# Performance work log

Hardware: AMD Instinct MI355X
Metric: run time of the kernel (lower is better)

The kernel has to match this reference:

```python
import jax, jax.numpy as jnp
import numpy as np

NUM_LEVELS = 4
CODEBOOK_SIZE = 256
DIM = 128
B = 262144


def setup_inputs() -> dict:
    key = jax.random.key(0)
    kx, kc = jax.random.split(key)
    x = jax.random.normal(kx, (B, DIM), dtype=jnp.float32)
    codebooks = jax.random.normal(kc, (NUM_LEVELS, CODEBOOK_SIZE, DIM), dtype=jnp.float32)
    return {"x": x, "codebooks": codebooks}


def reference(x, codebooks):
    # Residual quantization: per level, nearest codebook entry (L2), gather,
    # accumulate recon, subtract from residual.
    residual = x
    recon = jnp.zeros_like(x)
    codes = []
    for l in range(NUM_LEVELS):
        cb = codebooks[l]  # (K, D)
        # argmin of ||r - c||^2 == argmin of -2 r.c + ||c||^2 (drop ||r||^2 term)
        dist = -2.0 * (residual @ cb.T) + jnp.sum(cb * cb, axis=-1)  # (B, K)
        idx = jnp.argmin(dist, axis=1)  # (B,)
        codes.append(idx)
        selected = cb[idx]  # (B, D)
        recon = recon + selected
        residual = residual - selected
    codes = jnp.stack(codes, axis=1)  # (B, num_levels)
    return recon, codes
```

## Files before the change

kernel.cpp:

```cpp
#include <hip/hip_runtime.h>
#include <float.h>

#define NLVL  4
#define KCB   256
#define DIMD  128
#define NROWS 262144
#define WROWS 16
#define MARGIN 0.5f
#define WLCAP 256
#define RING  8
#define ADV   6

typedef _Float16 half8  __attribute__((ext_vector_type(8)));
typedef float    floatx4 __attribute__((ext_vector_type(4)));

#define WSYNC() asm volatile("s_waitcnt lgkmcnt(0)" ::: "memory")
#define VMW(N)  asm volatile("s_waitcnt vmcnt(" #N ")" ::: "memory")

__device__ __forceinline__ void glds16(const void* g, void* l) {
    __builtin_amdgcn_global_load_lds(
        (const __attribute__((address_space(1))) unsigned int*)g,
        (__attribute__((address_space(3))) unsigned int*)l, 16, 0, 0);
}

__global__ __launch_bounds__(256) void rq_prep_kernel(const float* __restrict__ cb,
                                                      float* __restrict__ c2,
                                                      _Float16* __restrict__ cbh) {
    int e = blockIdx.x * 256 + threadIdx.x;
    const float4* p = (const float4*)(cb + (size_t)e * DIMD);
    _Float16* ho = cbh + (size_t)e * DIMD;
    float s = 0.f;
#pragma unroll
    for (int k = 0; k < DIMD / 4; ++k) {
        float4 v = p[k];
        s = fmaf(v.x, v.x, s);
        s = fmaf(v.y, v.y, s);
        s = fmaf(v.z, v.z, s);
        s = fmaf(v.w, v.w, s);
        ho[4 * k + 0] = (_Float16)v.x;
        ho[4 * k + 1] = (_Float16)v.y;
        ho[4 * k + 2] = (_Float16)v.z;
        ho[4 * k + 3] = (_Float16)v.w;
    }
    c2[e] = s;
}

__global__ __launch_bounds__(64, 3) void rq_main_kernel(const float* __restrict__ x,
                                                        const float* __restrict__ cb,
                                                        const float* __restrict__ c2g,
                                                        const _Float16* __restrict__ cbh,
                                                        float* __restrict__ out) {
    __shared__ __align__(16) char ring[RING * 1024];
    __shared__ unsigned int wl[WLCAP];
    __shared__ unsigned long long refine_key[WROWS];
    __shared__ int codes_lds[WROWS][4];
    __shared__ int wl_cnt;

    const int lane = threadIdx.x;
    const int q    = lane >> 4;
    const int c    = lane & 15;
    const int rowW = blockIdx.x * WROWS;
    const int lane_off = ((lane >> 2) << 8) | ((lane & 3) << 4);
    const char* cbh_b = (const char*)cbh;

#pragma unroll
    for (int g = 0; g < ADV; ++g) {
        const char* src = cbh_b + ((g >> 6) << 16) + (((g & 63) >> 2) << 12)
                        + ((g & 3) << 6) + lane_off;
        glds16(src, ring + ((g & (RING - 1)) << 10));
    }

    float res_[32];
#pragma unroll
    for (int s = 0; s < 4; ++s) {
        const float* px = x + (size_t)(rowW + c) * DIMD + s * 32 + q * 8;
        float4 u = *(const float4*)px;
        float4 v = *(const float4*)(px + 4);
        res_[s*8+0]=u.x; res_[s*8+1]=u.y; res_[s*8+2]=u.z; res_[s*8+3]=u.w;
        res_[s*8+4]=v.x; res_[s*8+5]=v.y; res_[s*8+6]=v.z; res_[s*8+7]=v.w;
    }
    if (lane == 0) wl_cnt = 0;
    if (lane < WROWS) refine_key[lane] = ~0ULL;
    WSYNC();

    for (int l = 0; l < NLVL; ++l) {
        half8 a[4];
#pragma unroll
        for (int s = 0; s < 4; ++s)
#pragma unroll
            for (int j = 0; j < 8; ++j)
                a[s][j] = (_Float16)res_[s * 8 + j];

        floatx4 acc[16];
#pragma unroll
        for (int t = 0; t < 16; ++t) acc[t] = (floatx4){0.f, 0.f, 0.f, 0.f};

#pragma unroll
        for (int w = 0; w < 64; ++w) {
            if      (w <  59) VMW(5);
            else if (w == 59) VMW(4);
            else if (w == 60) VMW(3);
            else if (w == 61) VMW(2);
            else if (w == 62) VMW(1);
            else              VMW(0);
            half8 b = *(const half8*)(ring + ((w & (RING - 1)) << 10) + (c << 6) + (q << 4));
            if (l < NLVL - 1 || w < 64 - ADV) {
                int g2 = l * 64 + w + ADV;
                const char* src = cbh_b + ((g2 >> 6) << 16) + (((g2 & 63) >> 2) << 12)
                                + ((g2 & 3) << 6) + lane_off;
                glds16(src, ring + ((g2 & (RING - 1)) << 10));
            }
            acc[w >> 2] = __builtin_amdgcn_mfma_f32_16x16x32_f16(a[w & 3], b, acc[w >> 2], 0, 0, 0);
        }

        float c2v[16];
#pragma unroll
        for (int t = 0; t < 16; ++t) c2v[t] = c2g[l * KCB + t * 16 + c];

#pragma unroll
        for (int r = 0; r < 4; ++r) {
            float bv = FLT_MAX; int be = 0;
#pragma unroll
            for (int t = 0; t < 16; ++t) {
                float d = c2v[t] - 2.f * acc[t][r];
                if (d < bv) { bv = d; be = t * 16 + c; }
            }
#pragma unroll
            for (int m = 1; m < 16; m <<= 1) {
                float ov = __shfl_xor(bv, m);
                int   oe = __shfl_xor(be, m);
                if (ov < bv || (ov == bv && oe < be)) { bv = ov; be = oe; }
            }
            float thr = bv + MARGIN;
            int cnt = 0;
#pragma unroll
            for (int t = 0; t < 16; ++t)
                cnt += (c2v[t] - 2.f * acc[t][r]) <= thr;
#pragma unroll
            for (int m = 1; m < 16; m <<= 1) cnt += __shfl_xor(cnt, m);

            int row_m = q * 4 + r;
            if (c == 0) codes_lds[row_m][l] = be;
            if (cnt >= 2) {
#pragma unroll
                for (int t = 0; t < 16; ++t) {
                    float d = c2v[t] - 2.f * acc[t][r];
                    if (d <= thr) {
                        int slot = atomicAdd(&wl_cnt, 1);
                        if (slot < WLCAP)
                            wl[slot] = ((unsigned)row_m << 8) | (unsigned)(t * 16 + c);
                    }
                }
            }
        }
        WSYNC();

        int n = wl_cnt; if (n > WLCAP) n = WLCAP;
        for (int i = 0; i < n; ++i) {
            unsigned int it = wl[i];
            int row_m = (int)(it >> 8), e = (int)(it & 255u);
            bool act = (c == row_m);
            float d = 0.f;
            if (act) {
                const float* cc = cb + ((size_t)l * KCB + e) * DIMD + q * 8;
#pragma unroll
                for (int s = 0; s < 4; ++s) {
                    float4 u = *(const float4*)(cc + s * 32);
                    float4 v = *(const float4*)(cc + s * 32 + 4);
                    d = fmaf(res_[s*8+0], u.x, d); d = fmaf(res_[s*8+1], u.y, d);
                    d = fmaf(res_[s*8+2], u.z, d); d = fmaf(res_[s*8+3], u.w, d);
                    d = fmaf(res_[s*8+4], v.x, d); d = fmaf(res_[s*8+5], v.y, d);
                    d = fmaf(res_[s*8+6], v.z, d); d = fmaf(res_[s*8+7], v.w, d);
                }
            }
            d += __shfl_xor(d, 16);
            d += __shfl_xor(d, 32);
            if (act && q == 0) {
                float dist = c2g[l * KCB + e] - 2.f * d;
                unsigned int ob = __float_as_uint(dist);
                ob = (ob & 0x80000000u) ? ~ob : (ob | 0x80000000u);
                unsigned long long key = ((unsigned long long)ob << 32) | (unsigned int)e;
                atomicMin(&refine_key[row_m], key);
            }
        }
        WSYNC();

        {
            unsigned long long k = refine_key[c];
            int idx = (k != ~0ULL) ? (int)(k & 0xFFFFFFFFULL) : codes_lds[c][l];
            if (q == 0) codes_lds[c][l] = idx;
            const float* cbase = cb + ((size_t)l * KCB + idx) * DIMD + q * 8;
#pragma unroll
            for (int s = 0; s < 4; ++s) {
                float4 u = *(const float4*)(cbase + s * 32);
                float4 v = *(const float4*)(cbase + s * 32 + 4);
                res_[s*8+0] -= u.x; res_[s*8+1] -= u.y;
                res_[s*8+2] -= u.z; res_[s*8+3] -= u.w;
                res_[s*8+4] -= v.x; res_[s*8+5] -= v.y;
                res_[s*8+6] -= v.z; res_[s*8+7] -= v.w;
            }
        }
        if (lane == 0) wl_cnt = 0;
        if (lane < WROWS) refine_key[lane] = ~0ULL;
        WSYNC();
    }

#pragma unroll
    for (int s = 0; s < 4; ++s) {
        const float* px = x + (size_t)(rowW + c) * DIMD + s * 32 + q * 8;
        float4 u = *(const float4*)px;
        float4 v = *(const float4*)(px + 4);
        float4 o0, o1;
        o0.x = u.x - res_[s*8+0]; o0.y = u.y - res_[s*8+1];
        o0.z = u.z - res_[s*8+2]; o0.w = u.w - res_[s*8+3];
        o1.x = v.x - res_[s*8+4]; o1.y = v.y - res_[s*8+5];
        o1.z = v.z - res_[s*8+6]; o1.w = v.w - res_[s*8+7];
        float* po = out + (size_t)(rowW + c) * DIMD + s * 32 + q * 8;
        *(float4*)po = o0;
        *(float4*)(po + 4) = o1;
    }
    if (lane < WROWS) {
        float4 cd;
        cd.x = (float)codes_lds[lane][0];
        cd.y = (float)codes_lds[lane][1];
        cd.z = (float)codes_lds[lane][2];
        cd.w = (float)codes_lds[lane][3];
        ((float4*)(out + (size_t)NROWS * DIMD))[rowW + lane] = cd;
    }
}

extern "C" void kernel_launch(void* const* d_in, const int* in_sizes, int n_in,
                              void* d_out, int out_size, void* d_ws, size_t ws_size,
                              hipStream_t stream) {
    const float* x  = (const float*)d_in[0];
    const float* cb = (const float*)d_in[1];
    float* out = (float*)d_out;

    float*    c2  = (float*)d_ws;
    _Float16* cbh = (_Float16*)((char*)d_ws + 16384);

    rq_prep_kernel<<<NLVL * KCB / 256, 256, 0, stream>>>(cb, c2, cbh);
    rq_main_kernel<<<NROWS / WROWS, 64, 0, stream>>>(x, cb, c2, cbh, out);
}
```

Before: 511.1 us.

## Parallelize refinement across lanes via LDS residual copy; reorder codebook streaming

The refinement loop used to handle one worklist item per iteration, with 16 lanes active and shuffle reductions. It now gives each lane its own candidate, reading the row's residual from a padded LDS copy and doing a full 128-wide fp32 dot product per lane. This removes the serial per-item cost. The codebook ring layout and MFMA order change so each 1KB chunk covers one 16-entry tile at a K-slice, and the ring reads become contiguous per lane. Prefetch depth goes from 6 to 7, and the change adds LDS use plus extra residual stores per level.

Result: slower. 840.4 us (+64.4%).

```diff
diff --git a/kernel.cpp b/kernel.cpp
--- a/kernel.cpp
+++ b/kernel.cpp
@@ -9,7 +9,8 @@
 #define MARGIN 0.5f
 #define WLCAP 256
 #define RING  8
-#define ADV   6
+#define ADV   7
+#define RSTRIDE 132
 
 typedef _Float16 half8  __attribute__((ext_vector_type(8)));
 typedef float    floatx4 __attribute__((ext_vector_type(4)));
@@ -51,6 +52,7 @@
                                                         const _Float16* __restrict__ cbh,
                                                         float* __restrict__ out) {
     __shared__ __align__(16) char ring[RING * 1024];
+    __shared__ float res_lds[WROWS * RSTRIDE];
     __shared__ unsigned int wl[WLCAP];
     __shared__ unsigned long long refine_key[WROWS];
     __shared__ int codes_lds[WROWS][4];
@@ -60,13 +62,13 @@
     const int q    = lane >> 4;
     const int c    = lane & 15;
     const int rowW = blockIdx.x * WROWS;
-    const int lane_off = ((lane >> 2) << 8) | ((lane & 3) << 4);
+    const int lane_off = ((lane & 15) << 8) | ((lane >> 4) << 4);
     const char* cbh_b = (const char*)cbh;
 
 #pragma unroll
     for (int g = 0; g < ADV; ++g) {
-        const char* src = cbh_b + ((g >> 6) << 16) + (((g & 63) >> 2) << 12)
-                        + ((g & 3) << 6) + lane_off;
+        const char* src = cbh_b + ((g >> 6) << 16) + ((g & 15) << 12)
+                        + (((g & 63) >> 4) << 6) + lane_off;
         glds16(src, ring + ((g & (RING - 1)) << 10));
     }
 
@@ -79,6 +81,13 @@
         res_[s*8+0]=u.x; res_[s*8+1]=u.y; res_[s*8+2]=u.z; res_[s*8+3]=u.w;
         res_[s*8+4]=v.x; res_[s*8+5]=v.y; res_[s*8+6]=v.z; res_[s*8+7]=v.w;
     }
+#pragma unroll
+    for (int s = 0; s < 4; ++s) {
+        *(float4*)&res_lds[c * RSTRIDE + s * 32 + q * 8] =
+            (float4){res_[s*8+0], res_[s*8+1], res_[s*8+2], res_[s*8+3]};
+        *(float4*)&res_lds[c * RSTRIDE + s * 32 + q * 8 + 4] =
+            (float4){res_[s*8+4], res_[s*8+5], res_[s*8+6], res_[s*8+7]};
+    }
     if (lane == 0) wl_cnt = 0;
     if (lane < WROWS) refine_key[lane] = ~0ULL;
     WSYNC();
@@ -97,20 +106,21 @@
 
 #pragma unroll
         for (int w = 0; w < 64; ++w) {
-            if      (w <  59) VMW(5);
+            if      (w <  58) VMW(6);
+            else if (w == 58) VMW(5);
             else if (w == 59) VMW(4);
             else if (w == 60) VMW(3);
             else if (w == 61) VMW(2);
             else if (w == 62) VMW(1);
             else              VMW(0);
-            half8 b = *(const half8*)(ring + ((w & (RING - 1)) << 10) + (c << 6) + (q << 4));
+            half8 b = *(const half8*)(ring + ((w & (RING - 1)) << 10) + (lane << 4));
             if (l < NLVL - 1 || w < 64 - ADV) {
                 int g2 = l * 64 + w + ADV;
-                const char* src = cbh_b + ((g2 >> 6) << 16) + (((g2 & 63) >> 2) << 12)
-                                + ((g2 & 3) << 6) + lane_off;
+                const char* src = cbh_b + ((g2 >> 6) << 16) + ((g2 & 15) << 12)
+                                + (((g2 & 63) >> 4) << 6) + lane_off;
                 glds16(src, ring + ((g2 & (RING - 1)) << 10));
             }
-            acc[w >> 2] = __builtin_amdgcn_mfma_f32_16x16x32_f16(a[w & 3], b, acc[w >> 2], 0, 0, 0);
+            acc[w & 15] = __builtin_amdgcn_mfma_f32_16x16x32_f16(a[w >> 4], b, acc[w & 15], 0, 0, 0);
         }
 
         float c2v[16];
@@ -156,32 +166,26 @@
         WSYNC();
 
         int n = wl_cnt; if (n > WLCAP) n = WLCAP;
-        for (int i = 0; i < n; ++i) {
+        for (int i = lane; i < n; i += 64) {
             unsigned int it = wl[i];
             int row_m = (int)(it >> 8), e = (int)(it & 255u);
-            bool act = (c == row_m);
+            const float* rr = &res_lds[row_m * RSTRIDE];
+            const float* cc = cb + ((size_t)l * KCB + e) * DIMD;
             float d = 0.f;
-            if (act) {
-                const float* cc = cb + ((size_t)l * KCB + e) * DIMD + q * 8;
-#pragma unroll
-                for (int s = 0; s < 4; ++s) {
-                    float4 u = *(const float4*)(cc + s * 32);
-                    float4 v = *(const float4*)(cc + s * 32 + 4);
-                    d = fmaf(res_[s*8+0], u.x, d); d = fmaf(res_[s*8+1], u.y, d);
-                    d = fmaf(res_[s*8+2], u.z, d); d = fmaf(res_[s*8+3], u.w, d);
-                    d = fmaf(res_[s*8+4], v.x, d); d = fmaf(res_[s*8+5], v.y, d);
-                    d = fmaf(res_[s*8+6], v.z, d); d = fmaf(res_[s*8+7], v.w, d);
-                }
-            }
-            d += __shfl_xor(d, 16);
-            d += __shfl_xor(d, 32);
-            if (act && q == 0) {
-                float dist = c2g[l * KCB + e] - 2.f * d;
-                unsigned int ob = __float_as_uint(dist);
-                ob = (ob & 0x80000000u) ? ~ob : (ob | 0x80000000u);
-                unsigned long long key = ((unsigned long long)ob << 32) | (unsigned int)e;
-                atomicMin(&refine_key[row_m], key);
-            }
+#pragma unroll
+            for (int k = 0; k < DIMD / 4; ++k) {
+                float4 rv = *(const float4*)(rr + 4 * k);
+                float4 cv = *(const float4*)(cc + 4 * k);
+                d = fmaf(rv.x, cv.x, d);
+                d = fmaf(rv.y, cv.y, d);
+                d = fmaf(rv.z, cv.z, d);
+                d = fmaf(rv.w, cv.w, d);
+            }
+            float dist = c2g[l * KCB + e] - 2.f * d;
+            unsigned int ob = __float_as_uint(dist);
+            ob = (ob & 0x80000000u) ? ~ob : (ob | 0x80000000u);
+            unsigned long long key = ((unsigned long long)ob << 32) | (unsigned int)e;
+            atomicMin(&refine_key[row_m], key);
         }
         WSYNC();
 
@@ -198,6 +202,15 @@
                 res_[s*8+2] -= u.z; res_[s*8+3] -= u.w;
                 res_[s*8+4] -= v.x; res_[s*8+5] -= v.y;
                 res_[s*8+6] -= v.z; res_[s*8+7] -= v.w;
+            }
+            if (l < NLVL - 1) {
+#pragma unroll
+                for (int s = 0; s < 4; ++s) {
+                    *(float4*)&res_lds[c * RSTRIDE + s * 32 + q * 8] =
+                        (float4){res_[s*8+0], res_[s*8+1], res_[s*8+2], res_[s*8+3]};
+                    *(float4*)&res_lds[c * RSTRIDE + s * 32 + q * 8 + 4] =
+                        (float4){res_[s*8+4], res_[s*8+5], res_[s*8+6], res_[s*8+7]};
+                }
             }
         }
         if (lane == 0) wl_cnt = 0;
```

## Use per-row refine worklists, register-held codes, and reordered codebook prefetch

Applied to the files above, without the earlier changes.

Replaces the single shared worklist, which was serialized over all rows, with per-row worklists. Each lane group now refines its own row in parallel, keeping the running minimum in registers instead of using LDS atomicMin. Codes are kept in registers rather than LDS, and the level loop is fully unrolled. The codebook prefetch order and ring lane mapping are changed so the B fragments read contiguously, and the prefetch distance grows from 6 to 7. Risks are a per-row cap of 24 that can drop candidates, plus higher register pressure from unrolling.

New measurement: 802.3 us. 57.0% more time.

```diff
diff --git a/kernel.cpp b/kernel.cpp
--- a/kernel.cpp
+++ b/kernel.cpp
@@ -7,9 +7,9 @@
 #define NROWS 262144
 #define WROWS 16
 #define MARGIN 0.5f
-#define WLCAP 256
+#define WLROW 24
 #define RING  8
-#define ADV   6
+#define ADV   7
 
 typedef _Float16 half8  __attribute__((ext_vector_type(8)));
 typedef float    floatx4 __attribute__((ext_vector_type(4)));
@@ -51,22 +51,20 @@
                                                         const _Float16* __restrict__ cbh,
                                                         float* __restrict__ out) {
     __shared__ __align__(16) char ring[RING * 1024];
-    __shared__ unsigned int wl[WLCAP];
-    __shared__ unsigned long long refine_key[WROWS];
-    __shared__ int codes_lds[WROWS][4];
-    __shared__ int wl_cnt;
+    __shared__ unsigned int wl_row[WROWS][WLROW];
+    __shared__ int wl_cnt_row[WROWS];
 
     const int lane = threadIdx.x;
     const int q    = lane >> 4;
     const int c    = lane & 15;
     const int rowW = blockIdx.x * WROWS;
-    const int lane_off = ((lane >> 2) << 8) | ((lane & 3) << 4);
+    const int lane_off = ((lane & 15) << 8) | ((lane >> 4) << 4);
     const char* cbh_b = (const char*)cbh;
 
 #pragma unroll
     for (int g = 0; g < ADV; ++g) {
-        const char* src = cbh_b + ((g >> 6) << 16) + (((g & 63) >> 2) << 12)
-                        + ((g & 3) << 6) + lane_off;
+        const char* src = cbh_b + ((g >> 6) << 16) + ((g & 15) << 12)
+                        + (((g & 63) >> 4) << 6) + lane_off;
         glds16(src, ring + ((g & (RING - 1)) << 10));
     }
 
@@ -79,10 +77,12 @@
         res_[s*8+0]=u.x; res_[s*8+1]=u.y; res_[s*8+2]=u.z; res_[s*8+3]=u.w;
         res_[s*8+4]=v.x; res_[s*8+5]=v.y; res_[s*8+6]=v.z; res_[s*8+7]=v.w;
     }
-    if (lane == 0) wl_cnt = 0;
-    if (lane < WROWS) refine_key[lane] = ~0ULL;
+    if (lane < WROWS) wl_cnt_row[lane] = 0;
     WSYNC();
 
+    int code0 = 0, code1 = 0, code2 = 0, code3 = 0;
+
+#pragma unroll
     for (int l = 0; l < NLVL; ++l) {
         half8 a[4];
 #pragma unroll
@@ -97,26 +97,32 @@
 
 #pragma unroll
         for (int w = 0; w < 64; ++w) {
-            if      (w <  59) VMW(5);
-            else if (w == 59) VMW(4);
-            else if (w == 60) VMW(3);
-            else if (w == 61) VMW(2);
-            else if (w == 62) VMW(1);
-            else              VMW(0);
-            half8 b = *(const half8*)(ring + ((w & (RING - 1)) << 10) + (c << 6) + (q << 4));
+            if (l == NLVL - 1) {
+                if      (w <  58) VMW(6);
+                else if (w == 58) VMW(5);
+                else if (w == 59) VMW(4);
+                else if (w == 60) VMW(3);
+                else if (w == 61) VMW(2);
+                else if (w == 62) VMW(1);
+                else              VMW(0);
+            } else {
+                VMW(6);
+            }
+            half8 b = *(const half8*)(ring + ((w & (RING - 1)) << 10) + (lane << 4));
             if (l < NLVL - 1 || w < 64 - ADV) {
                 int g2 = l * 64 + w + ADV;
-                const char* src = cbh_b + ((g2 >> 6) << 16) + (((g2 & 63) >> 2) << 12)
-                                + ((g2 & 3) << 6) + lane_off;
+                const char* src = cbh_b + ((g2 >> 6) << 16) + ((g2 & 15) << 12)
+                                + (((g2 & 63) >> 4) << 6) + lane_off;
                 glds16(src, ring + ((g2 & (RING - 1)) << 10));
             }
-            acc[w >> 2] = __builtin_amdgcn_mfma_f32_16x16x32_f16(a[w & 3], b, acc[w >> 2], 0, 0, 0);
+            acc[w & 15] = __builtin_amdgcn_mfma_f32_16x16x32_f16(a[w >> 4], b, acc[w & 15], 0, 0, 0);
         }
 
         float c2v[16];
 #pragma unroll
         for (int t = 0; t < 16; ++t) c2v[t] = c2g[l * KCB + t * 16 + c];
 
+        int be0 = 0, be1 = 0, be2 = 0, be3 = 0;
 #pragma unroll
         for (int r = 0; r < 4; ++r) {
             float bv = FLT_MAX; int be = 0;
@@ -131,6 +137,11 @@
                 int   oe = __shfl_xor(be, m);
                 if (ov < bv || (ov == bv && oe < be)) { bv = ov; be = oe; }
             }
+            if      (r == 0) be0 = be;
+            else if (r == 1) be1 = be;
+            else if (r == 2) be2 = be;
+            else             be3 = be;
+
             float thr = bv + MARGIN;
             int cnt = 0;
 #pragma unroll
@@ -140,55 +151,60 @@
             for (int m = 1; m < 16; m <<= 1) cnt += __shfl_xor(cnt, m);
 
             int row_m = q * 4 + r;
-            if (c == 0) codes_lds[row_m][l] = be;
             if (cnt >= 2) {
 #pragma unroll
                 for (int t = 0; t < 16; ++t) {
                     float d = c2v[t] - 2.f * acc[t][r];
                     if (d <= thr) {
-                        int slot = atomicAdd(&wl_cnt, 1);
-                        if (slot < WLCAP)
-                            wl[slot] = ((unsigned)row_m << 8) | (unsigned)(t * 16 + c);
+                        int slot = atomicAdd(&wl_cnt_row[row_m], 1);
+                        if (slot < WLROW)
+                            wl_row[row_m][slot] = (unsigned)(t * 16 + c);
                     }
                 }
             }
         }
         WSYNC();
 
-        int n = wl_cnt; if (n > WLCAP) n = WLCAP;
-        for (int i = 0; i < n; ++i) {
-            unsigned int it = wl[i];
-            int row_m = (int)(it >> 8), e = (int)(it & 255u);
-            bool act = (c == row_m);
+        int src_l = ((c >> 2) << 4) | c;
+        int f0 = __shfl(be0, src_l), f1 = __shfl(be1, src_l);
+        int f2 = __shfl(be2, src_l), f3 = __shfl(be3, src_l);
+        int rsel = c & 3;
+        int se = f0;
+        se = (rsel == 1) ? f1 : se;
+        se = (rsel == 2) ? f2 : se;
+        se = (rsel == 3) ? f3 : se;
+
+        unsigned long long bk = ~0ULL;
+        int nc = wl_cnt_row[c]; if (nc > WLROW) nc = WLROW;
+        for (int i = 0; i < nc; ++i) {
+            int e = (int)wl_row[c][i];
+            const float* cc = cb + ((size_t)l * KCB + e) * DIMD;
             float d = 0.f;
-            if (act) {
-                const float* cc = cb + ((size_t)l * KCB + e) * DIMD + q * 8;
-#pragma unroll
-                for (int s = 0; s < 4; ++s) {
-                    float4 u = *(const float4*)(cc + s * 32);
-                    float4 v = *(const float4*)(cc + s * 32 + 4);
-                    d = fmaf(res_[s*8+0], u.x, d); d = fmaf(res_[s*8+1], u.y, d);
-                    d = fmaf(res_[s*8+2], u.z, d); d = fmaf(res_[s*8+3], u.w, d);
-                    d = fmaf(res_[s*8+4], v.x, d); d = fmaf(res_[s*8+5], v.y, d);
-                    d = fmaf(res_[s*8+6], v.z, d); d = fmaf(res_[s*8+7], v.w, d);
-                }
+#pragma unroll
+            for (int s = 0; s < 4; ++s) {
+                const float* cp = cc + s * 32 + q * 8;
+                float4 u = *(const float4*)cp;
+                float4 v = *(const float4*)(cp + 4);
+                d = fmaf(res_[s*8+0], u.x, d); d = fmaf(res_[s*8+1], u.y, d);
+                d = fmaf(res_[s*8+2], u.z, d); d = fmaf(res_[s*8+3], u.w, d);
+                d = fmaf(res_[s*8+4], v.x, d); d = fmaf(res_[s*8+5], v.y, d);
+                d = fmaf(res_[s*8+6], v.z, d); d = fmaf(res_[s*8+7], v.w, d);
             }
             d += __shfl_xor(d, 16);
             d += __shfl_xor(d, 32);
-            if (act && q == 0) {
-                float dist = c2g[l * KCB + e] - 2.f * d;
-                unsigned int ob = __float_as_uint(dist);
-                ob = (ob & 0x80000000u) ? ~ob : (ob | 0x80000000u);
-                unsigned long long key = ((unsigned long long)ob << 32) | (unsigned int)e;
-                atomicMin(&refine_key[row_m], key);
-            }
-        }
-        WSYNC();
+            float dist = c2g[l * KCB + e] - 2.f * d;
+            unsigned int ob = __float_as_uint(dist);
+            ob = (ob & 0x80000000u) ? ~ob : (ob | 0x80000000u);
+            unsigned long long key = ((unsigned long long)ob << 32) | (unsigned int)e;
+            bk = (key < bk) ? key : bk;
+        }
+        int idx = (bk != ~0ULL) ? (int)(bk & 0xFFFFFFFFULL) : se;
+        if      (l == 0) code0 = idx;
+        else if (l == 1) code1 = idx;
+        else if (l == 2) code2 = idx;
+        else             code3 = idx;
 
         {
-            unsigned long long k = refine_key[c];
-            int idx = (k != ~0ULL) ? (int)(k & 0xFFFFFFFFULL) : codes_lds[c][l];
-            if (q == 0) codes_lds[c][l] = idx;
             const float* cbase = cb + ((size_t)l * KCB + idx) * DIMD + q * 8;
 #pragma unroll
             for (int s = 0; s < 4; ++s) {
@@ -200,8 +216,7 @@
                 res_[s*8+6] -= v.z; res_[s*8+7] -= v.w;
             }
         }
-        if (lane == 0) wl_cnt = 0;
-        if (lane < WROWS) refine_key[lane] = ~0ULL;
+        if (lane < WROWS) wl_cnt_row[lane] = 0;
         WSYNC();
     }
 
@@ -221,10 +236,8 @@
     }
     if (lane < WROWS) {
         float4 cd;
-        cd.x = (float)codes_lds[lane][0];
-        cd.y = (float)codes_lds[lane][1];
-        cd.z = (float)codes_lds[lane][2];
-        cd.w = (float)codes_lds[lane][3];
+        cd.x = (float)code0; cd.y = (float)code1;
+        cd.z = (float)code2; cd.w = (float)code3;
         ((float4*)(out + (size_t)NROWS * DIMD))[rowW + lane] = cd;
     }
 }
```
